# Performance work log

Hardware: AMD Instinct MI355X
Metric: run time of the kernel (lower is better)

## Reference

```python
import jax, jax.numpy as jnp
import numpy as np

NUM_FEATURES = 10000
EMBED_DIM = 64
BATCH = 16384


def setup_inputs() -> dict:
    key = jax.random.key(0)
    k1, k2 = jax.random.split(key)
    # binary multi-hot indicator matrix [B, F]
    multi_hot = jax.random.randint(k1, (BATCH, NUM_FEATURES), 0, 2, dtype=jnp.int32)
    # xavier_uniform init: bound = sqrt(6 / (fan_in + fan_out))
    bound = float(np.sqrt(6.0 / (NUM_FEATURES + EMBED_DIM)))
    embed_matrix = jax.random.uniform(
        k2, (NUM_FEATURES, EMBED_DIM), minval=-bound, maxval=bound, dtype=jnp.float32
    )
    return {"multi_hot": multi_hot, "embed_matrix": embed_matrix}


def reference(multi_hot, embed_matrix):
    # multi_hot.float() @ embed_matrix  -> [B, D]
    return jnp.matmul(multi_hot.astype(embed_matrix.dtype), embed_matrix)
```

## Files before the change

### kernel.cpp

```cpp
#include <hip/hip_runtime.h>


typedef int    int4v   __attribute__((ext_vector_type(4)));
typedef float  float4v __attribute__((ext_vector_type(4)));
typedef float  f32x4   __attribute__((ext_vector_type(4)));
typedef short  bf16x8  __attribute__((ext_vector_type(8)));
typedef unsigned int uint4v __attribute__((ext_vector_type(4)));
typedef unsigned int uint2v __attribute__((ext_vector_type(2)));

constexpr int M_DIM   = 16384;
constexpr int K_DIM   = 10000;
constexpr int N_DIM   = 64;
constexpr int BM      = 32;
constexpr int BK      = 64;
constexpr int NCH_PAD = 158;
constexpr int KSTRIDE = 144;

__device__ __forceinline__ unsigned f2bf(float x) {
    unsigned u = __builtin_bit_cast(unsigned, x);
    u += 0x7FFFu + ((u >> 16) & 1u);
    return u >> 16;
}

struct ARegs { int4v   q0, q1, q2, q3; };
struct BRegs { float4v r0, r1, r2, r3; };

__global__ __launch_bounds__(256, 2) void mhe_gemm(
        const int* __restrict__ mh, const float* __restrict__ em,
        float* __restrict__ out) {
    __shared__ __align__(16) char lds[2][64 * KSTRIDE];

    const int tid  = threadIdx.x;
    const int lane = tid & 63;
    const int wv   = tid >> 6;
    const int wm   = wv >> 1;
    const int wn   = wv & 1;
    const int row0 = (int)blockIdx.x * BM;

    const int g8 = (lane >> 4) << 3;
    const long long arow = row0 + wm * 16 + (lane & 15);
    const int* __restrict__ ap = mh + arow * (long long)K_DIM;

    const int kg = tid >> 4;
    const int ng = tid & 15;

    f32x4 acc0 = {0.f, 0.f, 0.f, 0.f};
    f32x4 acc1 = {0.f, 0.f, 0.f, 0.f};

    char* const lds0 = &lds[0][0];
    char* const lds1 = &lds[1][0];

    auto loadA = [&](ARegs& a, int f0) {
        if (f0 + BK <= K_DIM) {
            const int4v* p0 = (const int4v*)(ap + f0 + g8);
            const int4v* p1 = (const int4v*)(ap + f0 + 32 + g8);
            a.q0 = p0[0]; a.q1 = p0[1];
            a.q2 = p1[0]; a.q3 = p1[1];
        } else {
            a.q0 = {}; a.q1 = {}; a.q2 = {}; a.q3 = {};
            const int b0 = f0 + g8;
            if (b0      < K_DIM) a.q0 = *(const int4v*)(ap + b0);
            if (b0 + 4  < K_DIM) a.q1 = *(const int4v*)(ap + b0 + 4);
            if (b0 + 32 < K_DIM) a.q2 = *(const int4v*)(ap + b0 + 32);
            if (b0 + 36 < K_DIM) a.q3 = *(const int4v*)(ap + b0 + 36);
        }
    };

    auto loadB = [&](BRegs& b, int f0) {
        const int r = f0 + kg * 4;
        if (f0 + BK <= K_DIM) {
            const float* p = em + r * N_DIM + ng * 4;
            b.r0 = *(const float4v*)(p);
            b.r1 = *(const float4v*)(p + N_DIM);
            b.r2 = *(const float4v*)(p + 2 * N_DIM);
            b.r3 = *(const float4v*)(p + 3 * N_DIM);
        } else {
            b.r0 = {}; b.r1 = {}; b.r2 = {}; b.r3 = {};
            if (r + 0 < K_DIM) b.r0 = *(const float4v*)(em + (r + 0) * N_DIM + ng * 4);
            if (r + 1 < K_DIM) b.r1 = *(const float4v*)(em + (r + 1) * N_DIM + ng * 4);
            if (r + 2 < K_DIM) b.r2 = *(const float4v*)(em + (r + 2) * N_DIM + ng * 4);
            if (r + 3 < K_DIM) b.r3 = *(const float4v*)(em + (r + 3) * N_DIM + ng * 4);
        }
    };

    auto stageB = [&](const BRegs& b, char* buf) {
        char* wp = buf + (ng * 4) * KSTRIDE + kg * 8;
        #pragma unroll
        for (int i = 0; i < 4; ++i) {
            uint2v w = { f2bf(b.r0[i]) | (f2bf(b.r1[i]) << 16),
                         f2bf(b.r2[i]) | (f2bf(b.r3[i]) << 16) };
            *(uint2v*)(wp + i * KSTRIDE) = w;
        }
    };

    auto packA = [&](int4v qa, int4v qb) -> bf16x8 {
        uint4v w;
        w[0] = (unsigned)(qa[0] | (qa[1] << 16)) * 0x3F80u;
        w[1] = (unsigned)(qa[2] | (qa[3] << 16)) * 0x3F80u;
        w[2] = (unsigned)(qb[0] | (qb[1] << 16)) * 0x3F80u;
        w[3] = (unsigned)(qb[2] | (qb[3] << 16)) * 0x3F80u;
        return __builtin_bit_cast(bf16x8, w);
    };

    const int rboff = (wn * 32 + (lane & 15)) * KSTRIDE + ((lane >> 4) << 4);

    auto compute = [&](const ARegs& a, const char* buf) {
        bf16x8 af0 = packA(a.q0, a.q1);
        bf16x8 af1 = packA(a.q2, a.q3);
        const char* rb = buf + rboff;
        bf16x8 b00 = *(const bf16x8*)(rb);
        bf16x8 b01 = *(const bf16x8*)(rb + 64);
        bf16x8 b10 = *(const bf16x8*)(rb + 16 * KSTRIDE);
        bf16x8 b11 = *(const bf16x8*)(rb + 16 * KSTRIDE + 64);
        acc0 = __builtin_amdgcn_mfma_f32_16x16x32_bf16(af0, b00, acc0, 0, 0, 0);
        acc1 = __builtin_amdgcn_mfma_f32_16x16x32_bf16(af0, b10, acc1, 0, 0, 0);
        acc0 = __builtin_amdgcn_mfma_f32_16x16x32_bf16(af1, b01, acc0, 0, 0, 0);
        acc1 = __builtin_amdgcn_mfma_f32_16x16x32_bf16(af1, b11, acc1, 0, 0, 0);
    };

    ARegs aC, aN; BRegs bC, bN;
    loadA(aC, 0); loadB(bC, 0);
    stageB(bC, lds0);
    __syncthreads();

    for (int t = 0; t < NCH_PAD; t += 2) {
        loadA(aN, (t + 1) * BK); loadB(bN, (t + 1) * BK);
        compute(aC, lds0);
        stageB(bN, lds1);
        __syncthreads();
        loadA(aC, (t + 2) * BK); loadB(bC, (t + 2) * BK);
        compute(aN, lds1);
        stageB(bC, lds0);
        __syncthreads();
    }

    const int crow = row0 + wm * 16 + ((lane >> 4) << 2);
    const int ccol = wn * 32 + (lane & 15);
    #pragma unroll
    for (int i = 0; i < 4; ++i) {
        out[(crow + i) * N_DIM + ccol]      = acc0[i];
        out[(crow + i) * N_DIM + ccol + 16] = acc1[i];
    }
}

extern "C" void kernel_launch(void* const* d_in, const int* in_sizes, int n_in,
                              void* d_out, int out_size, void* d_ws, size_t ws_size,
                              hipStream_t stream) {
    const int*   mh  = (const int*)d_in[0];
    const float* em  = (const float*)d_in[1];
    float*       out = (float*)d_out;
    (void)in_sizes; (void)n_in; (void)out_size; (void)d_ws; (void)ws_size;

    dim3 grid(M_DIM / BM);
    dim3 block(256);
    mhe_gemm<<<grid, block, 0, stream>>>(mh, em, out);
}
```

Measured before the change: 232.3 us.

## Split K four ways with atomics and pre-transposed bf16 weights in workspace

A prep kernel now converts the embedding matrix once into a transposed, padded bf16 layout in workspace and zeroes the output. The main kernel drops LDS staging and block barriers: each wave owns a 32-row tile over one quarter of K, reads B fragments straight from global memory, and accumulates into the output with atomic adds. A is read with nontemporal loads. The aim is more parallelism (four times as many waves) and no per-block conversion or sync overhead, at the cost of an extra launch, atomic traffic, and redundant B reads served from cache.

```diff
diff --git a/kernel.cpp b/kernel.cpp
--- a/kernel.cpp
+++ b/kernel.cpp
@@ -6,15 +6,16 @@
 typedef float  f32x4   __attribute__((ext_vector_type(4)));
 typedef short  bf16x8  __attribute__((ext_vector_type(8)));
 typedef unsigned int uint4v __attribute__((ext_vector_type(4)));
-typedef unsigned int uint2v __attribute__((ext_vector_type(2)));
 
 constexpr int M_DIM   = 16384;
 constexpr int K_DIM   = 10000;
 constexpr int N_DIM   = 64;
-constexpr int BM      = 32;
 constexpr int BK      = 64;
-constexpr int NCH_PAD = 158;
-constexpr int KSTRIDE = 144;
+constexpr int NCH_PAD = 160;
+constexpr int KPAD    = NCH_PAD * BK;
+constexpr int SPLIT   = 4;
+constexpr int NCH_SEG = NCH_PAD / SPLIT;
+constexpr int WM      = 32;
 
 __device__ __forceinline__ unsigned f2bf(float x) {
     unsigned u = __builtin_bit_cast(unsigned, x);
@@ -22,125 +23,151 @@
     return u >> 16;
 }
 
-struct ARegs { int4v   q0, q1, q2, q3; };
-struct BRegs { float4v r0, r1, r2, r3; };
+__global__ __launch_bounds__(256) void prep(const float* __restrict__ em,
+                                            unsigned short* __restrict__ bt,
+                                            float* __restrict__ out) {
+    const int tid = threadIdx.x;
+    const int b   = blockIdx.x;
+    if (b < NCH_PAD) {
+        __shared__ float t[64][65];
+        const int k0 = b * 64;
+        #pragma unroll
+        for (int rep = 0; rep < 16; ++rep) {
+            const int idx = rep * 256 + tid;
+            const int k = idx >> 6, n = idx & 63;
+            float v = 0.f;
+            if (k0 + k < K_DIM) v = em[(k0 + k) * N_DIM + n];
+            t[n][k] = v;
+        }
+        __syncthreads();
+        const int n  = tid >> 2;
+        const int kk = (tid & 3) * 16;
+        unsigned w[8];
+        #pragma unroll
+        for (int j = 0; j < 8; ++j)
+            w[j] = f2bf(t[n][kk + 2 * j]) | (f2bf(t[n][kk + 2 * j + 1]) << 16);
+        uint4v lo = {w[0], w[1], w[2], w[3]};
+        uint4v hi = {w[4], w[5], w[6], w[7]};
+        uint4v* dst = (uint4v*)(bt + (long long)n * KPAD + k0 + kk);
+        dst[0] = lo; dst[1] = hi;
+    } else {
+        const int b2 = b - NCH_PAD;
+        float4v z = {0.f, 0.f, 0.f, 0.f};
+        float4v* p = (float4v*)out;
+        const int base = b2 * 256 + tid;
+        #pragma unroll
+        for (int i = 0; i < 4; ++i) p[base + i * 65536] = z;
+    }
+}
+
+struct ARegs { int4v q0, q1, q2, q3; };
+struct BF    { bf16x8 f[4][2]; };
 
 __global__ __launch_bounds__(256, 2) void mhe_gemm(
-        const int* __restrict__ mh, const float* __restrict__ em,
+        const int* __restrict__ mh, const unsigned short* __restrict__ bt,
         float* __restrict__ out) {
-    __shared__ __align__(16) char lds[2][64 * KSTRIDE];
-
     const int tid  = threadIdx.x;
     const int lane = tid & 63;
     const int wv   = tid >> 6;
-    const int wm   = wv >> 1;
-    const int wn   = wv & 1;
-    const int row0 = (int)blockIdx.x * BM;
+    const int w    = (int)blockIdx.x * 4 + wv;
+    const int seg  = w >> 9;
+    const int rowblk = w & 511;
+    const int row0 = rowblk * WM;
+    const int c0   = seg * NCH_SEG;
 
     const int g8 = (lane >> 4) << 3;
-    const long long arow = row0 + wm * 16 + (lane & 15);
-    const int* __restrict__ ap = mh + arow * (long long)K_DIM;
+    const int* __restrict__ ap0 = mh + (long long)(row0 + (lane & 15)) * K_DIM;
+    const int* __restrict__ ap1 = ap0 + (long long)16 * K_DIM;
 
-    const int kg = tid >> 4;
-    const int ng = tid & 15;
+    const unsigned short* __restrict__ bpn[4];
+    #pragma unroll
+    for (int nt = 0; nt < 4; ++nt)
+        bpn[nt] = bt + (long long)(nt * 16 + (lane & 15)) * KPAD + g8;
 
-    f32x4 acc0 = {0.f, 0.f, 0.f, 0.f};
-    f32x4 acc1 = {0.f, 0.f, 0.f, 0.f};
+    f32x4 acc[2][4] = {};
 
-    char* const lds0 = &lds[0][0];
-    char* const lds1 = &lds[1][0];
+    auto packA = [&](int4v qa, int4v qb) -> bf16x8 {
+        uint4v x;
+        x[0] = (unsigned)(qa[0] | (qa[1] << 16)) * 0x3F80u;
+        x[1] = (unsigned)(qa[2] | (qa[3] << 16)) * 0x3F80u;
+        x[2] = (unsigned)(qb[0] | (qb[1] << 16)) * 0x3F80u;
+        x[3] = (unsigned)(qb[2] | (qb[3] << 16)) * 0x3F80u;
+        return __builtin_bit_cast(bf16x8, x);
+    };
 
-    auto loadA = [&](ARegs& a, int f0) {
+    auto loadAB = [&](ARegs& x0, ARegs& x1, BF& bb, int c) {
+        const int f0 = c * BK;
         if (f0 + BK <= K_DIM) {
-            const int4v* p0 = (const int4v*)(ap + f0 + g8);
-            const int4v* p1 = (const int4v*)(ap + f0 + 32 + g8);
-            a.q0 = p0[0]; a.q1 = p0[1];
-            a.q2 = p1[0]; a.q3 = p1[1];
+            const int4v* p0 = (const int4v*)(ap0 + f0 + g8);
+            const int4v* p1 = (const int4v*)(ap0 + f0 + 32 + g8);
+            const int4v* p2 = (const int4v*)(ap1 + f0 + g8);
+            const int4v* p3 = (const int4v*)(ap1 + f0 + 32 + g8);
+            x0.q0 = __builtin_nontemporal_load(p0);
+            x0.q1 = __builtin_nontemporal_load(p0 + 1);
+            x0.q2 = __builtin_nontemporal_load(p1);
+            x0.q3 = __builtin_nontemporal_load(p1 + 1);
+            x1.q0 = __builtin_nontemporal_load(p2);
+            x1.q1 = __builtin_nontemporal_load(p2 + 1);
+            x1.q2 = __builtin_nontemporal_load(p3);
+            x1.q3 = __builtin_nontemporal_load(p3 + 1);
         } else {
-            a.q0 = {}; a.q1 = {}; a.q2 = {}; a.q3 = {};
+            x0.q0 = {}; x0.q1 = {}; x0.q2 = {}; x0.q3 = {};
+            x1.q0 = {}; x1.q1 = {}; x1.q2 = {}; x1.q3 = {};
             const int b0 = f0 + g8;
-            if (b0      < K_DIM) a.q0 = *(const int4v*)(ap + b0);
-            if (b0 + 4  < K_DIM) a.q1 = *(const int4v*)(ap + b0 + 4);
-            if (b0 + 32 < K_DIM) a.q2 = *(const int4v*)(ap + b0 + 32);
-            if (b0 + 36 < K_DIM) a.q3 = *(const int4v*)(ap + b0 + 36);
+            if (b0      < K_DIM) { x0.q0 = *(const int4v*)(ap0 + b0);
+                                   x1.q0 = *(const int4v*)(ap1 + b0); }
+            if (b0 + 4  < K_DIM) { x0.q1 = *(const int4v*)(ap0 + b0 + 4);
+                                   x1.q1 = *(const int4v*)(ap1 + b0 + 4); }
+            if (b0 + 32 < K_DIM) { x0.q2 = *(const int4v*)(ap0 + b0 + 32);
+                                   x1.q2 = *(const int4v*)(ap1 + b0 + 32); }
+            if (b0 + 36 < K_DIM) { x0.q3 = *(const int4v*)(ap0 + b0 + 36);
+                                   x1.q3 = *(const int4v*)(ap1 + b0 + 36); }
+        }
+        #pragma unroll
+        for (int nt = 0; nt < 4; ++nt) {
+            bb.f[nt][0] = *(const bf16x8*)(bpn[nt] + f0);
+            bb.f[nt][1] = *(const bf16x8*)(bpn[nt] + f0 + 32);
         }
     };
 
-    auto loadB = [&](BRegs& b, int f0) {
-        const int r = f0 + kg * 4;
-        if (f0 + BK <= K_DIM) {
-            const float* p = em + r * N_DIM + ng * 4;
-            b.r0 = *(const float4v*)(p);
-            b.r1 = *(const float4v*)(p + N_DIM);
-            b.r2 = *(const float4v*)(p + 2 * N_DIM);
-            b.r3 = *(const float4v*)(p + 3 * N_DIM);
-        } else {
-            b.r0 = {}; b.r1 = {}; b.r2 = {}; b.r3 = {};
-            if (r + 0 < K_DIM) b.r0 = *(const float4v*)(em + (r + 0) * N_DIM + ng * 4);
-            if (r + 1 < K_DIM) b.r1 = *(const float4v*)(em + (r + 1) * N_DIM + ng * 4);
-            if (r + 2 < K_DIM) b.r2 = *(const float4v*)(em + (r + 2) * N_DIM + ng * 4);
-            if (r + 3 < K_DIM) b.r3 = *(const float4v*)(em + (r + 3) * N_DIM + ng * 4);
+    auto compute = [&](const ARegs& x0, const ARegs& x1, const BF& bb) {
+        bf16x8 a00 = packA(x0.q0, x0.q1);
+        bf16x8 a01 = packA(x0.q2, x0.q3);
+        bf16x8 a10 = packA(x1.q0, x1.q1);
+        bf16x8 a11 = packA(x1.q2, x1.q3);
+        #pragma unroll
+        for (int nt = 0; nt < 4; ++nt) {
+            acc[0][nt] = __builtin_amdgcn_mfma_f32_16x16x32_bf16(a00, bb.f[nt][0], acc[0][nt], 0, 0, 0);
+            acc[0][nt] = __builtin_amdgcn_mfma_f32_16x16x32_bf16(a01, bb.f[nt][1], acc[0][nt], 0, 0, 0);
+            acc[1][nt] = __builtin_amdgcn_mfma_f32_16x16x32_bf16(a10, bb.f[nt][0], acc[1][nt], 0, 0, 0);
+            acc[1][nt] = __builtin_amdgcn_mfma_f32_16x16x32_bf16(a11, bb.f[nt][1], acc[1][nt], 0, 0, 0);
         }
     };
 
-    auto stageB = [&](const BRegs& b, char* buf) {
-        char* wp = buf + (ng * 4) * KSTRIDE + kg * 8;
+    ARegs a0A, a1A, a0B, a1B;
+    BF bA, bB;
+    loadAB(a0A, a1A, bA, c0);
+    int c = c0;
+    for (; c + 2 < c0 + NCH_SEG; c += 2) {
+        loadAB(a0B, a1B, bB, c + 1);
+        compute(a0A, a1A, bA);
+        loadAB(a0A, a1A, bA, c + 2);
+        compute(a0B, a1B, bB);
+    }
+    loadAB(a0B, a1B, bB, c + 1);
+    compute(a0A, a1A, bA);
+    compute(a0B, a1B, bB);
+
+    const int crow = row0 + ((lane >> 4) << 2);
+    const int ccol = lane & 15;
+    #pragma unroll
+    for (int mt = 0; mt < 2; ++mt)
         #pragma unroll
-        for (int i = 0; i < 4; ++i) {
-            uint2v w = { f2bf(b.r0[i]) | (f2bf(b.r1[i]) << 16),
-                         f2bf(b.r2[i]) | (f2bf(b.r3[i]) << 16) };
-            *(uint2v*)(wp + i * KSTRIDE) = w;
-        }
-    };
-
-    auto packA = [&](int4v qa, int4v qb) -> bf16x8 {
-        uint4v w;
-        w[0] = (unsigned)(qa[0] | (qa[1] << 16)) * 0x3F80u;
-        w[1] = (unsigned)(qa[2] | (qa[3] << 16)) * 0x3F80u;
-        w[2] = (unsigned)(qb[0] | (qb[1] << 16)) * 0x3F80u;
-        w[3] = (unsigned)(qb[2] | (qb[3] << 16)) * 0x3F80u;
-        return __builtin_bit_cast(bf16x8, w);
-    };
-
-    const int rboff = (wn * 32 + (lane & 15)) * KSTRIDE + ((lane >> 4) << 4);
-
-    auto compute = [&](const ARegs& a, const char* buf) {
-        bf16x8 af0 = packA(a.q0, a.q1);
-        bf16x8 af1 = packA(a.q2, a.q3);
-        const char* rb = buf + rboff;
-        bf16x8 b00 = *(const bf16x8*)(rb);
-        bf16x8 b01 = *(const bf16x8*)(rb + 64);
-        bf16x8 b10 = *(const bf16x8*)(rb + 16 * KSTRIDE);
-        bf16x8 b11 = *(const bf16x8*)(rb + 16 * KSTRIDE + 64);
-        acc0 = __builtin_amdgcn_mfma_f32_16x16x32_bf16(af0, b00, acc0, 0, 0, 0);
-        acc1 = __builtin_amdgcn_mfma_f32_16x16x32_bf16(af0, b10, acc1, 0, 0, 0);
-        acc0 = __builtin_amdgcn_mfma_f32_16x16x32_bf16(af1, b01, acc0, 0, 0, 0);
-        acc1 = __builtin_amdgcn_mfma_f32_16x16x32_bf16(af1, b11, acc1, 0, 0, 0);
-    };
-
-    ARegs aC, aN; BRegs bC, bN;
-    loadA(aC, 0); loadB(bC, 0);
-    stageB(bC, lds0);
-    __syncthreads();
-
-    for (int t = 0; t < NCH_PAD; t += 2) {
-        loadA(aN, (t + 1) * BK); loadB(bN, (t + 1) * BK);
-        compute(aC, lds0);
-        stageB(bN, lds1);
-        __syncthreads();
-        loadA(aC, (t + 2) * BK); loadB(bC, (t + 2) * BK);
-        compute(aN, lds1);
-        stageB(bC, lds0);
-        __syncthreads();
-    }
-
-    const int crow = row0 + wm * 16 + ((lane >> 4) << 2);
-    const int ccol = wn * 32 + (lane & 15);
-    #pragma unroll
-    for (int i = 0; i < 4; ++i) {
-        out[(crow + i) * N_DIM + ccol]      = acc0[i];
-        out[(crow + i) * N_DIM + ccol + 16] = acc1[i];
-    }
+        for (int nt = 0; nt < 4; ++nt)
+            #pragma unroll
+            for (int i = 0; i < 4; ++i)
+                unsafeAtomicAdd(&out[(long long)(crow + mt * 16 + i) * N_DIM + nt * 16 + ccol],
+                                acc[mt][nt][i]);
 }
 
 extern "C" void kernel_launch(void* const* d_in, const int* in_sizes, int n_in,
@@ -149,9 +176,9 @@
     const int*   mh  = (const int*)d_in[0];
     const float* em  = (const float*)d_in[1];
     float*       out = (float*)d_out;
-    (void)in_sizes; (void)n_in; (void)out_size; (void)d_ws; (void)ws_size;
+    unsigned short* bt = (unsigned short*)d_ws;
+    (void)in_sizes; (void)n_in; (void)out_size; (void)ws_size;
 
-    dim3 grid(M_DIM / BM);
-    dim3 block(256);
-    mhe_gemm<<<grid, block, 0, stream>>>(mh, em, out);
+    prep<<<dim3(NCH_PAD + 256), dim3(256), 0, stream>>>(em, bt, out);
+    mhe_gemm<<<dim3((M_DIM / WM) * SPLIT / 4), dim3(256), 0, stream>>>(mh, bt, out);
 }
```

Result: no change. 235.6 us (+1.4%).
